# Kernel tuning notes

Measured on AMD Instinct MI355X. Metric: run time of the kernel, lower is better.

Reference implementation:

```python
import jax, jax.numpy as jnp
import numpy as np

B, S, D = 2, 2048, 1024
H, DK, DV = 16, 64, 64
N_WINDOW = 256
LN_EPS = 1e-5


def setup_inputs() -> dict:
    key = jax.random.key(0)
    ks = jax.random.split(key, 8)
    sc = 0.02
    return {
        "Q": jax.random.normal(ks[0], (B, S, D), jnp.float32),
        "K": jax.random.normal(ks[1], (B, S, D), jnp.float32),
        "V": jax.random.normal(ks[2], (B, S, D), jnp.float32),
        "Wq": jax.random.normal(ks[3], (D, H * DK), jnp.float32) * sc,
        "bq": jnp.zeros((H * DK,), jnp.float32),
        "Wk": jax.random.normal(ks[4], (D, H * DK), jnp.float32) * sc,
        "bk": jnp.zeros((H * DK,), jnp.float32),
        "Wv": jax.random.normal(ks[5], (D, H * DV), jnp.float32) * sc,
        "bv": jnp.zeros((H * DV,), jnp.float32),
        "Wo": jax.random.normal(ks[6], (H * DV, D), jnp.float32) * sc,
        "bo": jnp.zeros((D,), jnp.float32),
        "gamma": jnp.ones((D,), jnp.float32),
        "beta": jnp.zeros((D,), jnp.float32),
    }


def reference(Q, K, V, Wq, bq, Wk, bk, Wv, bv, Wo, bo, gamma, beta):
    b, s, _ = Q.shape
    # QKV projections -> [b, s, h, d]
    q = (Q @ Wq + bq).reshape(b, s, H, DK)
    k = (K @ Wk + bk).reshape(b, s, H, DK)
    v = (V @ Wv + bv).reshape(b, s, H, DV)
    # scores [b, h, i, j]
    scores = jnp.einsum("bihd,bjhd->bhij", q, k) / np.sqrt(DK).astype(np.float32)
    # sliding-window band mask |i - j| < N_WINDOW (mask=True path)
    idx = jnp.arange(s)
    band = jnp.abs(idx[:, None] - idx[None, :]) < N_WINDOW  # [s, s]
    scores = jnp.where(band[None, None], scores, -jnp.inf)
    attn = jax.nn.softmax(scores, axis=-1)
    ctx = jnp.einsum("bhij,bjhd->bihd", attn, v).reshape(b, s, H * DV)
    out = ctx @ Wo + bo
    # residual + LayerNorm over last dim
    x = out + Q
    mu = jnp.mean(x, axis=-1, keepdims=True)
    var = jnp.mean(jnp.square(x - mu), axis=-1, keepdims=True)
    y = (x - mu) * jax.lax.rsqrt(var + LN_EPS) * gamma + beta
    return y, attn
```

## Files before the change

kernel.cpp:

```cpp
#include <hip/hip_runtime.h>
#include <hip/hip_bf16.h>

#define BB 2
#define SS 2048
#define HH 16
#define LN_EPS 1e-5f
#define LOG2E 1.44269504088896f

typedef __attribute__((ext_vector_type(8))) short short8;
typedef __attribute__((ext_vector_type(4))) float floatx4;

#define EXP2F(x) __builtin_amdgcn_exp2f(x)

__device__ __forceinline__ ushort f2b(float f) {
    union { float f; unsigned u; } x; x.f = f;
    unsigned u = x.u;
    return (ushort)((u + 0x7FFFu + ((u >> 16) & 1u)) >> 16);
}
__device__ __forceinline__ float b2f(ushort u) {
    union { unsigned u; float f; } x; x.u = ((unsigned)u) << 16;
    return x.f;
}

__global__ __launch_bounds__(256) void wtrans(
    const float* __restrict__ W0, const float* __restrict__ W1,
    const float* __restrict__ W2, const float* __restrict__ W3,
    ushort* __restrict__ T0, ushort* __restrict__ T1,
    ushort* __restrict__ T2, ushort* __restrict__ T3)
{
    const int z = blockIdx.z;
    const float* W = z == 0 ? W0 : z == 1 ? W1 : z == 2 ? W2 : W3;
    ushort* T = z == 0 ? T0 : z == 1 ? T1 : z == 2 ? T2 : T3;
    const float scale = (z == 0) ? 0.125f : 1.0f;
    __shared__ float ts[32][33];
    const int k0 = blockIdx.y * 32, n0 = blockIdx.x * 32;
    const int r = threadIdx.x >> 3, c4 = (threadIdx.x & 7) * 4;
    float4 v = *(const float4*)&W[(size_t)(k0 + r) * 1024 + n0 + c4];
    ts[r][c4 + 0] = v.x; ts[r][c4 + 1] = v.y; ts[r][c4 + 2] = v.z; ts[r][c4 + 3] = v.w;
    __syncthreads();
    ushort4 o;
    o.x = f2b(ts[c4 + 0][r] * scale); o.y = f2b(ts[c4 + 1][r] * scale);
    o.z = f2b(ts[c4 + 2][r] * scale); o.w = f2b(ts[c4 + 3][r] * scale);
    *(ushort4*)&T[(size_t)(n0 + r) * 1024 + k0 + c4] = o;
}

__device__ __forceinline__ void gemm_body(
    const float* Af, const ushort* Ab, const ushort* __restrict__ Bt,
    const float* __restrict__ bias, float bscale,
    float* Cf, ushort* Cb, int m0, int n0)
{
    __shared__ ushort As[128 * 40];
    __shared__ ushort Bs[64 * 40];
    const int t = threadIdx.x;
    const int l = t & 63;
    const int w = t >> 6;
    const int wm = w >> 1, wn = w & 1;

    floatx4 acc[4][2] = {};
    const int r0 = t >> 2;
    const int c0 = t & 3;

    for (int k0 = 0; k0 < 1024; k0 += 32) {
        short8 a0, a1;
        if (Af) {
            const float* p0 = &Af[(size_t)(m0 + r0) * 1024 + k0 + c0 * 8];
            const float* p1 = &Af[(size_t)(m0 + r0 + 64) * 1024 + k0 + c0 * 8];
            float4 x0 = *(const float4*)p0, y0 = *(const float4*)(p0 + 4);
            float4 x1 = *(const float4*)p1, y1 = *(const float4*)(p1 + 4);
            a0[0] = (short)f2b(x0.x); a0[1] = (short)f2b(x0.y); a0[2] = (short)f2b(x0.z); a0[3] = (short)f2b(x0.w);
            a0[4] = (short)f2b(y0.x); a0[5] = (short)f2b(y0.y); a0[6] = (short)f2b(y0.z); a0[7] = (short)f2b(y0.w);
            a1[0] = (short)f2b(x1.x); a1[1] = (short)f2b(x1.y); a1[2] = (short)f2b(x1.z); a1[3] = (short)f2b(x1.w);
            a1[4] = (short)f2b(y1.x); a1[5] = (short)f2b(y1.y); a1[6] = (short)f2b(y1.z); a1[7] = (short)f2b(y1.w);
        } else {
            a0 = *(const short8*)&Ab[(size_t)(m0 + r0) * 1024 + k0 + c0 * 8];
            a1 = *(const short8*)&Ab[(size_t)(m0 + r0 + 64) * 1024 + k0 + c0 * 8];
        }
        short8 b0 = *(const short8*)&Bt[(size_t)(n0 + r0) * 1024 + k0 + c0 * 8];

        __syncthreads();
        *(short8*)&As[r0 * 40 + c0 * 8] = a0;
        *(short8*)&As[(r0 + 64) * 40 + c0 * 8] = a1;
        *(short8*)&Bs[r0 * 40 + c0 * 8] = b0;
        __syncthreads();

        short8 af[4], bf[2];
#pragma unroll
        for (int m = 0; m < 4; ++m)
            af[m] = *(const short8*)&As[(wm * 64 + m * 16 + (l & 15)) * 40 + (l >> 4) * 8];
#pragma unroll
        for (int n = 0; n < 2; ++n)
            bf[n] = *(const short8*)&Bs[(wn * 32 + n * 16 + (l & 15)) * 40 + (l >> 4) * 8];
#pragma unroll
        for (int m = 0; m < 4; ++m)
#pragma unroll
            for (int n = 0; n < 2; ++n)
                acc[m][n] = __builtin_amdgcn_mfma_f32_16x16x32_bf16(af[m], bf[n], acc[m][n], 0, 0, 0);
    }

    const int cr = (l >> 4) * 4;
    const int cc = l & 15;
#pragma unroll
    for (int n = 0; n < 2; ++n) {
        int col = n0 + wn * 32 + n * 16 + cc;
        float bv = bias[col] * bscale;
#pragma unroll
        for (int m = 0; m < 4; ++m) {
            int row = m0 + wm * 64 + m * 16 + cr;
#pragma unroll
            for (int j = 0; j < 4; ++j) {
                float v = acc[m][n][j] + bv;
                if (Cf) Cf[(size_t)(row + j) * 1024 + col] = v;
                else    Cb[(size_t)(row + j) * 1024 + col] = f2b(v);
            }
        }
    }
}

__device__ __forceinline__ void swz_mn(int& m0, int& n0) {
    int bid = blockIdx.x + (blockIdx.y << 4);
    int xcd = bid & 7, idx = bid >> 3;
    m0 = (xcd * 4 + (idx & 3)) * 128;
    n0 = (idx >> 2) * 64;
}

__global__ __launch_bounds__(256) void gemm_qkv(
    const float* __restrict__ Q, const float* __restrict__ K, const float* __restrict__ V,
    const ushort* __restrict__ Wqt, const ushort* __restrict__ Wkt, const ushort* __restrict__ Wvt,
    const float* __restrict__ bq, const float* __restrict__ bk, const float* __restrict__ bv,
    ushort* __restrict__ qp, ushort* __restrict__ kp, ushort* __restrict__ vp)
{
    const int z = blockIdx.z;
    const float* A = z == 0 ? Q : z == 1 ? K : V;
    const ushort* Bt = z == 0 ? Wqt : z == 1 ? Wkt : Wvt;
    const float* bias = z == 0 ? bq : z == 1 ? bk : bv;
    ushort* C = z == 0 ? qp : z == 1 ? kp : vp;
    float bscale = (z == 0) ? 0.125f : 1.0f;
    int m0, n0; swz_mn(m0, n0);
    gemm_body(A, nullptr, Bt, bias, bscale, nullptr, C, m0, n0);
}

__global__ __launch_bounds__(256) void gemm_obf(
    const ushort* __restrict__ ctxb, const ushort* __restrict__ Wot,
    const float* __restrict__ bo, float* __restrict__ op)
{
    int m0, n0; swz_mn(m0, n0);
    gemm_body(nullptr, ctxb, Wot, bo, 1.0f, op, nullptr, m0, n0);
}

__global__ __launch_bounds__(256, 4) void attn_mfma(
    const ushort* __restrict__ qb, const ushort* __restrict__ kb, const ushort* __restrict__ vb,
    float* __restrict__ attn, ushort* __restrict__ ctxb)
{
    __shared__ alignas(16) ushort Ks[64 * 72];
    __shared__ alignas(16) ushort Vt[64 * 72];
    __shared__ alignas(16) ushort Pl[4][16 * 72];

    const int qblk = blockIdx.x, h = blockIdx.y, b = blockIdx.z;
    const int i0 = qblk * 64;
    const int t = threadIdx.x;
    const int w = t >> 6, l = t & 63;
    const int g = l >> 4, c = l & 15;
    const int ibase = i0 + w * 16;

    const int jstart = max(0, i0 - 256);
    const int jend = min(SS, i0 + 64 + 256);

    const size_t qoff = (size_t)(b * SS + ibase + c) * 1024 + h * 64 + g * 8;
    short8 aq0 = *(const short8*)&qb[qoff];
    short8 aq1 = *(const short8*)&qb[qoff + 32];

    const int krow = t >> 2, kd0 = (t & 3) * 16;
    const int vj0 = (t & 31) * 2, vd0 = (t >> 5) * 8;

    float m[4] = {-3e38f, -3e38f, -3e38f, -3e38f};
    float ll[4] = {0.f, 0.f, 0.f, 0.f};

    for (int jt = jstart; jt < jend; jt += 64) {
        __syncthreads();
        {
            const ushort* kr = &kb[(size_t)(b * SS + jt + krow) * 1024 + h * 64 + kd0];
            short8 k0 = *(const short8*)kr;
            short8 k1 = *(const short8*)(kr + 8);
            *(short8*)&Ks[krow * 72 + kd0] = k0;
            *(short8*)&Ks[krow * 72 + kd0 + 8] = k1;
        }
        __syncthreads();
        floatx4 s[4] = {};
#pragma unroll
        for (int u = 0; u < 4; ++u) {
            short8 b0 = *(const short8*)&Ks[(u * 16 + c) * 72 + g * 8];
            short8 b1 = *(const short8*)&Ks[(u * 16 + c) * 72 + 32 + g * 8];
            s[u] = __builtin_amdgcn_mfma_f32_16x16x32_bf16(aq0, b0, s[u], 0, 0, 0);
            s[u] = __builtin_amdgcn_mfma_f32_16x16x32_bf16(aq1, b1, s[u], 0, 0, 0);
        }
        const bool full = (jt >= ibase - 240) && (jt <= ibase + 192);
#pragma unroll
        for (int r = 0; r < 4; ++r) {
            float v0 = s[0][r] * LOG2E, v1 = s[1][r] * LOG2E,
                  v2 = s[2][r] * LOG2E, v3 = s[3][r] * LOG2E;
            if (!full) {
                const int i = ibase + g * 4 + r;
                const int j0 = jt + c;
                if ((unsigned)(i - j0 + 255) >= 511u)        v0 = -3e38f;
                if ((unsigned)(i - (j0 + 16) + 255) >= 511u) v1 = -3e38f;
                if ((unsigned)(i - (j0 + 32) + 255) >= 511u) v2 = -3e38f;
                if ((unsigned)(i - (j0 + 48) + 255) >= 511u) v3 = -3e38f;
            }
            float tmax = fmaxf(fmaxf(v0, v1), fmaxf(v2, v3));
            float mn = fmaxf(m[r], tmax);
            float sc_ = EXP2F(m[r] - mn);
            float add = EXP2F(v0 - mn) + EXP2F(v1 - mn)
                      + EXP2F(v2 - mn) + EXP2F(v3 - mn);
            ll[r] = ll[r] * sc_ + add;
            m[r] = mn;
        }
    }

    float M[4], invL[4];
#pragma unroll
    for (int r = 0; r < 4; ++r) {
        float mm = m[r];
        mm = fmaxf(mm, __shfl_xor(mm, 1));
        mm = fmaxf(mm, __shfl_xor(mm, 2));
        mm = fmaxf(mm, __shfl_xor(mm, 4));
        mm = fmaxf(mm, __shfl_xor(mm, 8));
        float la = ll[r] * EXP2F(m[r] - mm);
        la += __shfl_xor(la, 1);
        la += __shfl_xor(la, 2);
        la += __shfl_xor(la, 4);
        la += __shfl_xor(la, 8);
        M[r] = mm;
        invL[r] = 1.0f / la;
    }

    floatx4 ctx[4] = {};
    for (int jt = jstart; jt < jend; jt += 64) {
        __syncthreads();
        {
            const ushort* kr = &kb[(size_t)(b * SS + jt + krow) * 1024 + h * 64 + kd0];
            short8 k0 = *(const short8*)kr;
            short8 k1 = *(const short8*)(kr + 8);
            *(short8*)&Ks[krow * 72 + kd0] = k0;
            *(short8*)&Ks[krow * 72 + kd0 + 8] = k1;
        }
        {
            const ushort* vr = &vb[(size_t)(b * SS + jt + vj0) * 1024 + h * 64 + vd0];
            short8 v0 = *(const short8*)vr;
            short8 v1 = *(const short8*)(vr + 1024);
#pragma unroll
            for (int e = 0; e < 8; ++e) {
                ushort2 pr;
                pr.x = (ushort)v0[e];
                pr.y = (ushort)v1[e];
                *(ushort2*)&Vt[(vd0 + e) * 72 + vj0] = pr;
            }
        }
        __syncthreads();
        floatx4 s[4] = {};
#pragma unroll
        for (int u = 0; u < 4; ++u) {
            short8 b0 = *(const short8*)&Ks[(u * 16 + c) * 72 + g * 8];
            short8 b1 = *(const short8*)&Ks[(u * 16 + c) * 72 + 32 + g * 8];
            s[u] = __builtin_amdgcn_mfma_f32_16x16x32_bf16(aq0, b0, s[u], 0, 0, 0);
            s[u] = __builtin_amdgcn_mfma_f32_16x16x32_bf16(aq1, b1, s[u], 0, 0, 0);
        }
        const bool full = (jt >= ibase - 240) && (jt <= ibase + 192);
#pragma unroll
        for (int u = 0; u < 4; ++u) {
#pragma unroll
            for (int r = 0; r < 4; ++r) {
                float v = s[u][r] * LOG2E;
                if (!full) {
                    const int i = ibase + g * 4 + r;
                    const int j = jt + u * 16 + c;
                    if ((unsigned)(i - j + 255) >= 511u) v = -3e38f;
                }
                float p = EXP2F(v - M[r]) * invL[r];
                Pl[w][(g * 4 + r) * 72 + u * 16 + c] = f2b(p);
            }
        }
#pragma unroll
        for (int it = 0; it < 4; ++it) {
            const int row = it * 4 + g;
            ushort4 pw = *(const ushort4*)&Pl[w][row * 72 + c * 4];
            floatx4 o;
            o[0] = b2f(pw.x); o[1] = b2f(pw.y); o[2] = b2f(pw.z); o[3] = b2f(pw.w);
            __builtin_nontemporal_store(o,
                (floatx4*)&attn[(size_t)(b * HH + h) * SS * SS + (size_t)(ibase + row) * SS + jt + c * 4]);
        }
#pragma unroll
        for (int jc = 0; jc < 2; ++jc) {
            short8 pa = *(const short8*)&Pl[w][c * 72 + jc * 32 + g * 8];
#pragma unroll
            for (int ds = 0; ds < 4; ++ds) {
                short8 bv_ = *(const short8*)&Vt[(ds * 16 + c) * 72 + jc * 32 + g * 8];
                ctx[ds] = __builtin_amdgcn_mfma_f32_16x16x32_bf16(pa, bv_, ctx[ds], 0, 0, 0);
            }
        }
    }

#pragma unroll
    for (int ds = 0; ds < 4; ++ds)
#pragma unroll
        for (int r = 0; r < 4; ++r)
            ctxb[(size_t)(b * SS + ibase + g * 4 + r) * 1024 + h * 64 + ds * 16 + c] = f2b(ctx[ds][r]);

    {
        float* ab = attn + (size_t)(b * HH + h) * SS * SS;
        const floatx4 z4 = {0.f, 0.f, 0.f, 0.f};
        const int g16 = t >> 4, c16 = t & 15;
#pragma unroll
        for (int rr = 0; rr < 4; ++rr) {
            float* rp = ab + (size_t)(i0 + g16 + rr * 16) * SS;
            for (int x = c16 * 4; x < jstart; x += 64)
                __builtin_nontemporal_store(z4, (floatx4*)&rp[x]);
            for (int x = jend + c16 * 4; x < SS; x += 64)
                __builtin_nontemporal_store(z4, (floatx4*)&rp[x]);
        }
    }
}

__global__ __launch_bounds__(256) void ln_kernel(
    const float* __restrict__ op, const float* __restrict__ Qin,
    const float* __restrict__ gamma, const float* __restrict__ beta,
    float* __restrict__ y)
{
    const int row = blockIdx.x;
    const int t = threadIdx.x;
    __shared__ float rs[4], rss[4];

    float4 o4 = *(const float4*)&op[(size_t)row * 1024 + t * 4];
    float4 q4 = *(const float4*)&Qin[(size_t)row * 1024 + t * 4];
    float x0 = o4.x + q4.x, x1 = o4.y + q4.y, x2 = o4.z + q4.z, x3 = o4.w + q4.w;
    float s = x0 + x1 + x2 + x3;
    float ss = x0 * x0 + x1 * x1 + x2 * x2 + x3 * x3;
#pragma unroll
    for (int off = 1; off < 64; off <<= 1) {
        s  += __shfl_xor(s, off, 64);
        ss += __shfl_xor(ss, off, 64);
    }
    int wid = t >> 6;
    if ((t & 63) == 0) { rs[wid] = s; rss[wid] = ss; }
    __syncthreads();
    s  = rs[0] + rs[1] + rs[2] + rs[3];
    ss = rss[0] + rss[1] + rss[2] + rss[3];
    float mu = s * (1.0f / 1024.0f);
    float var = ss * (1.0f / 1024.0f) - mu * mu;
    float rstd = rsqrtf(var + LN_EPS);
    float4 g4 = *(const float4*)&gamma[t * 4];
    float4 b4 = *(const float4*)&beta[t * 4];
    float4 o;
    o.x = (x0 - mu) * rstd * g4.x + b4.x;
    o.y = (x1 - mu) * rstd * g4.y + b4.y;
    o.z = (x2 - mu) * rstd * g4.z + b4.z;
    o.w = (x3 - mu) * rstd * g4.w + b4.w;
    *(float4*)&y[(size_t)row * 1024 + t * 4] = o;
}

extern "C" void kernel_launch(void* const* d_in, const int* in_sizes, int n_in,
                              void* d_out, int out_size, void* d_ws, size_t ws_size,
                              hipStream_t stream) {
    (void)in_sizes; (void)n_in; (void)out_size; (void)ws_size;
    const float* Q  = (const float*)d_in[0];
    const float* K  = (const float*)d_in[1];
    const float* V  = (const float*)d_in[2];
    const float* Wq = (const float*)d_in[3];
    const float* bq = (const float*)d_in[4];
    const float* Wk = (const float*)d_in[5];
    const float* bk = (const float*)d_in[6];
    const float* Wv = (const float*)d_in[7];
    const float* bv = (const float*)d_in[8];
    const float* Wo = (const float*)d_in[9];
    const float* bo = (const float*)d_in[10];
    const float* gamma = (const float*)d_in[11];
    const float* beta  = (const float*)d_in[12];

    float* y = (float*)d_out;
    float* attn = y + (size_t)BB * SS * 1024;

    float* op = (float*)d_ws;
    ushort* ub = (ushort*)(op + 4194304);
    ushort* qbp  = ub;
    ushort* kbp  = ub + (size_t)4194304;
    ushort* vbp  = ub + (size_t)2 * 4194304;
    ushort* ctxb = ub + (size_t)3 * 4194304;
    ushort* Wqt  = ub + (size_t)4 * 4194304;
    ushort* Wkt  = Wqt + 1048576;
    ushort* Wvt  = Wkt + 1048576;
    ushort* Wot  = Wvt + 1048576;

    wtrans<<<dim3(32, 32, 4), 256, 0, stream>>>(Wq, Wk, Wv, Wo, Wqt, Wkt, Wvt, Wot);
    gemm_qkv<<<dim3(16, 32, 3), 256, 0, stream>>>(Q, K, V, Wqt, Wkt, Wvt, bq, bk, bv, qbp, kbp, vbp);
    attn_mfma<<<dim3(SS / 64, HH, BB), 256, 0, stream>>>(qbp, kbp, vbp, attn, ctxb);
    gemm_obf<<<dim3(16, 32), 256, 0, stream>>>(ctxb, Wot, bo, op);
    ln_kernel<<<4096, 256, 0, stream>>>(op, Q, gamma, beta, y);
}
```

Measured before the change: 239.5 us.

## Pre-convert inputs to bf16, use direct global-to-LDS loads and 128x128 GEMM tiles

```diff
diff --git a/kernel.cpp b/kernel.cpp
--- a/kernel.cpp
+++ b/kernel.cpp
@@ -11,6 +11,9 @@
 typedef __attribute__((ext_vector_type(4))) float floatx4;
 
 #define EXP2F(x) __builtin_amdgcn_exp2f(x)
+#define GLOAD16(g, l) __builtin_amdgcn_global_load_lds( \
+    (const __attribute__((address_space(1))) void*)(g), \
+    (__attribute__((address_space(3))) void*)(l), 16, 0, 0)
 
 __device__ __forceinline__ ushort f2b(float f) {
     union { float f; unsigned u; } x; x.f = f;
@@ -20,6 +23,22 @@
 __device__ __forceinline__ float b2f(ushort u) {
     union { unsigned u; float f; } x; x.u = ((unsigned)u) << 16;
     return x.f;
+}
+
+__global__ __launch_bounds__(256) void to_bf16(
+    const float* __restrict__ X0, const float* __restrict__ X1, const float* __restrict__ X2,
+    ushort* __restrict__ Y0, ushort* __restrict__ Y1, ushort* __restrict__ Y2)
+{
+    const int z = blockIdx.z;
+    const float* X = z == 0 ? X0 : z == 1 ? X1 : X2;
+    ushort* Y = z == 0 ? Y0 : z == 1 ? Y1 : Y2;
+    const size_t i = ((size_t)blockIdx.x * 256 + threadIdx.x) * 8;
+    float4 a = *(const float4*)&X[i];
+    float4 b = *(const float4*)&X[i + 4];
+    short8 o;
+    o[0] = (short)f2b(a.x); o[1] = (short)f2b(a.y); o[2] = (short)f2b(a.z); o[3] = (short)f2b(a.w);
+    o[4] = (short)f2b(b.x); o[5] = (short)f2b(b.y); o[6] = (short)f2b(b.z); o[7] = (short)f2b(b.w);
+    *(short8*)&Y[i] = o;
 }
 
 __global__ __launch_bounds__(256) void wtrans(
@@ -45,63 +64,61 @@
 }
 
 __device__ __forceinline__ void gemm_body(
-    const float* Af, const ushort* Ab, const ushort* __restrict__ Bt,
+    const ushort* __restrict__ Ab, const ushort* __restrict__ Bt,
     const float* __restrict__ bias, float bscale,
     float* Cf, ushort* Cb, int m0, int n0)
 {
-    __shared__ ushort As[128 * 40];
-    __shared__ ushort Bs[64 * 40];
+    __shared__ ushort As[128 * 32];
+    __shared__ ushort Bs[128 * 32];
     const int t = threadIdx.x;
     const int l = t & 63;
     const int w = t >> 6;
     const int wm = w >> 1, wn = w & 1;
 
-    floatx4 acc[4][2] = {};
-    const int r0 = t >> 2;
-    const int c0 = t & 3;
+    floatx4 acc[4][4] = {};
+
+    const int i0c = w * 64 + l;
+    const int r0 = i0c >> 2, c0 = i0c & 3;
+    const int i1c = 256 + i0c;
+    const int r1 = i1c >> 2, c1 = i1c & 3;
+
+    const ushort* gA0 = &Ab[(size_t)(m0 + r0) * 1024 + c0 * 8];
+    const ushort* gA1 = &Ab[(size_t)(m0 + r1) * 1024 + c1 * 8];
+    const ushort* gB0 = &Bt[(size_t)(n0 + r0) * 1024 + c0 * 8];
+    const ushort* gB1 = &Bt[(size_t)(n0 + r1) * 1024 + c1 * 8];
+
+    char* lA = (char*)As;
+    char* lB = (char*)Bs;
+    const int d0 = (w * 64) * 16;
+    const int d1 = (256 + w * 64) * 16;
 
     for (int k0 = 0; k0 < 1024; k0 += 32) {
-        short8 a0, a1;
-        if (Af) {
-            const float* p0 = &Af[(size_t)(m0 + r0) * 1024 + k0 + c0 * 8];
-            const float* p1 = &Af[(size_t)(m0 + r0 + 64) * 1024 + k0 + c0 * 8];
-            float4 x0 = *(const float4*)p0, y0 = *(const float4*)(p0 + 4);
-            float4 x1 = *(const float4*)p1, y1 = *(const float4*)(p1 + 4);
-            a0[0] = (short)f2b(x0.x); a0[1] = (short)f2b(x0.y); a0[2] = (short)f2b(x0.z); a0[3] = (short)f2b(x0.w);
-            a0[4] = (short)f2b(y0.x); a0[5] = (short)f2b(y0.y); a0[6] = (short)f2b(y0.z); a0[7] = (short)f2b(y0.w);
-            a1[0] = (short)f2b(x1.x); a1[1] = (short)f2b(x1.y); a1[2] = (short)f2b(x1.z); a1[3] = (short)f2b(x1.w);
-            a1[4] = (short)f2b(y1.x); a1[5] = (short)f2b(y1.y); a1[6] = (short)f2b(y1.z); a1[7] = (short)f2b(y1.w);
-        } else {
-            a0 = *(const short8*)&Ab[(size_t)(m0 + r0) * 1024 + k0 + c0 * 8];
-            a1 = *(const short8*)&Ab[(size_t)(m0 + r0 + 64) * 1024 + k0 + c0 * 8];
-        }
-        short8 b0 = *(const short8*)&Bt[(size_t)(n0 + r0) * 1024 + k0 + c0 * 8];
-
-        __syncthreads();
-        *(short8*)&As[r0 * 40 + c0 * 8] = a0;
-        *(short8*)&As[(r0 + 64) * 40 + c0 * 8] = a1;
-        *(short8*)&Bs[r0 * 40 + c0 * 8] = b0;
-        __syncthreads();
-
-        short8 af[4], bf[2];
+        __syncthreads();
+        GLOAD16(gA0 + k0, lA + d0);
+        GLOAD16(gA1 + k0, lA + d1);
+        GLOAD16(gB0 + k0, lB + d0);
+        GLOAD16(gB1 + k0, lB + d1);
+        __syncthreads();
+
+        short8 af[4], bf[4];
 #pragma unroll
         for (int m = 0; m < 4; ++m)
-            af[m] = *(const short8*)&As[(wm * 64 + m * 16 + (l & 15)) * 40 + (l >> 4) * 8];
-#pragma unroll
-        for (int n = 0; n < 2; ++n)
-            bf[n] = *(const short8*)&Bs[(wn * 32 + n * 16 + (l & 15)) * 40 + (l >> 4) * 8];
+            af[m] = *(const short8*)&As[(wm * 64 + m * 16 + (l & 15)) * 32 + (l >> 4) * 8];
+#pragma unroll
+        for (int n = 0; n < 4; ++n)
+            bf[n] = *(const short8*)&Bs[(wn * 64 + n * 16 + (l & 15)) * 32 + (l >> 4) * 8];
 #pragma unroll
         for (int m = 0; m < 4; ++m)
 #pragma unroll
-            for (int n = 0; n < 2; ++n)
+            for (int n = 0; n < 4; ++n)
                 acc[m][n] = __builtin_amdgcn_mfma_f32_16x16x32_bf16(af[m], bf[n], acc[m][n], 0, 0, 0);
     }
 
     const int cr = (l >> 4) * 4;
     const int cc = l & 15;
 #pragma unroll
-    for (int n = 0; n < 2; ++n) {
-        int col = n0 + wn * 32 + n * 16 + cc;
+    for (int n = 0; n < 4; ++n) {
+        int col = n0 + wn * 64 + n * 16 + cc;
         float bv = bias[col] * bscale;
 #pragma unroll
         for (int m = 0; m < 4; ++m) {
@@ -117,26 +134,26 @@
 }
 
 __device__ __forceinline__ void swz_mn(int& m0, int& n0) {
-    int bid = blockIdx.x + (blockIdx.y << 4);
+    int bid = blockIdx.x + (blockIdx.y << 3);
     int xcd = bid & 7, idx = bid >> 3;
     m0 = (xcd * 4 + (idx & 3)) * 128;
-    n0 = (idx >> 2) * 64;
+    n0 = (idx >> 2) * 128;
 }
 
 __global__ __launch_bounds__(256) void gemm_qkv(
-    const float* __restrict__ Q, const float* __restrict__ K, const float* __restrict__ V,
+    const ushort* __restrict__ Xq, const ushort* __restrict__ Xk, const ushort* __restrict__ Xv,
     const ushort* __restrict__ Wqt, const ushort* __restrict__ Wkt, const ushort* __restrict__ Wvt,
     const float* __restrict__ bq, const float* __restrict__ bk, const float* __restrict__ bv,
     ushort* __restrict__ qp, ushort* __restrict__ kp, ushort* __restrict__ vp)
 {
     const int z = blockIdx.z;
-    const float* A = z == 0 ? Q : z == 1 ? K : V;
+    const ushort* A = z == 0 ? Xq : z == 1 ? Xk : Xv;
     const ushort* Bt = z == 0 ? Wqt : z == 1 ? Wkt : Wvt;
     const float* bias = z == 0 ? bq : z == 1 ? bk : bv;
     ushort* C = z == 0 ? qp : z == 1 ? kp : vp;
     float bscale = (z == 0) ? 0.125f : 1.0f;
     int m0, n0; swz_mn(m0, n0);
-    gemm_body(A, nullptr, Bt, bias, bscale, nullptr, C, m0, n0);
+    gemm_body(A, Bt, bias, bscale, nullptr, C, m0, n0);
 }
 
 __global__ __launch_bounds__(256) void gemm_obf(
@@ -144,7 +161,7 @@
     const float* __restrict__ bo, float* __restrict__ op)
 {
     int m0, n0; swz_mn(m0, n0);
-    gemm_body(nullptr, ctxb, Wot, bo, 1.0f, op, nullptr, m0, n0);
+    gemm_body(ctxb, Wot, bo, 1.0f, op, nullptr, m0, n0);
 }
 
 __global__ __launch_bounds__(256, 4) void attn_mfma(
@@ -378,20 +395,24 @@
     float* y = (float*)d_out;
     float* attn = y + (size_t)BB * SS * 1024;
 
-    float* op = (float*)d_ws;
-    ushort* ub = (ushort*)(op + 4194304);
-    ushort* qbp  = ub;
-    ushort* kbp  = ub + (size_t)4194304;
-    ushort* vbp  = ub + (size_t)2 * 4194304;
-    ushort* ctxb = ub + (size_t)3 * 4194304;
-    ushort* Wqt  = ub + (size_t)4 * 4194304;
-    ushort* Wkt  = Wqt + 1048576;
-    ushort* Wvt  = Wkt + 1048576;
-    ushort* Wot  = Wvt + 1048576;
-
+    char* base = (char*)d_ws;
+    float*  op   = (float*)base;
+    ushort* Xq   = (ushort*)base;
+    ushort* Xk   = (ushort*)(base + (size_t)8 * 1048576);
+    ushort* Xv   = (ushort*)(base + (size_t)16 * 1048576);
+    ushort* ctxb = (ushort*)(base + (size_t)16 * 1048576);
+    ushort* qbp  = (ushort*)(base + (size_t)24 * 1048576);
+    ushort* kbp  = (ushort*)(base + (size_t)32 * 1048576);
+    ushort* vbp  = (ushort*)(base + (size_t)40 * 1048576);
+    ushort* Wqt  = (ushort*)(base + (size_t)48 * 1048576);
+    ushort* Wkt  = (ushort*)(base + (size_t)50 * 1048576);
+    ushort* Wvt  = (ushort*)(base + (size_t)52 * 1048576);
+    ushort* Wot  = (ushort*)(base + (size_t)54 * 1048576);
+
+    to_bf16<<<dim3(2048, 1, 3), 256, 0, stream>>>(Q, K, V, Xq, Xk, Xv);
     wtrans<<<dim3(32, 32, 4), 256, 0, stream>>>(Wq, Wk, Wv, Wo, Wqt, Wkt, Wvt, Wot);
-    gemm_qkv<<<dim3(16, 32, 3), 256, 0, stream>>>(Q, K, V, Wqt, Wkt, Wvt, bq, bk, bv, qbp, kbp, vbp);
+    gemm_qkv<<<dim3(8, 32, 3), 256, 0, stream>>>(Xq, Xk, Xv, Wqt, Wkt, Wvt, bq, bk, bv, qbp, kbp, vbp);
     attn_mfma<<<dim3(SS / 64, HH, BB), 256, 0, stream>>>(qbp, kbp, vbp, attn, ctxb);
-    gemm_obf<<<dim3(16, 32), 256, 0, stream>>>(ctxb, Wot, bo, op);
+    gemm_obf<<<dim3(8, 32), 256, 0, stream>>>(ctxb, Wot, bo, op);
     ln_kernel<<<4096, 256, 0, stream>>>(op, Q, gamma, beta, y);
 }
```

Result: faster. 232.0 us (-3.1%).
